# Kernel tuning notes

Measured on AMD Instinct MI355X. Metric: run time of the kernel, lower is better.

The kernel has to match this reference:

```python
import jax, jax.numpy as jnp
import numpy as np

TEMPS = (0.02, 0.05, 0.2)
EPS = 1e-06


def _pairwise_dist_sq(x, y):
    # (N, M) squared L2 distances, clamped at 0 like the torch version
    dsq = (x * x).sum(-1)[:, None] + (y * y).sum(-1)[None, :] - 2.0 * (x @ y.T)
    return jnp.maximum(dsq, 0.0)


def reference(gen_features, pos_features, drift_scales):
    gen, pos = gen_features, pos_features
    N = gen.shape[0]
    # Distances are temperature-independent; compute once and reuse across temps.
    d_att = jnp.sqrt(_pairwise_dist_sq(gen, pos))  # (N_gen, N_pos)
    eye = jnp.eye(N, dtype=bool)
    dsq_rep = _pairwise_dist_sq(gen, gen)
    # diagonal gets masked to -inf in the logits anyway; replace 0 before sqrt for numerical safety
    d_rep = jnp.sqrt(jnp.where(eye, 1.0, dsq_rep))  # (N_gen, N_gen)

    drift_sum = jnp.zeros_like(gen)
    for i, T in enumerate(TEMPS):
        # attraction: sum_j softmax(-d/T)_ij * (pos_j - gen_i) == softmax @ pos - gen
        # (weights sum to 1 along axis=1, so the -gen_i term factors out)
        w_att = jax.nn.softmax(-d_att / T, axis=1)
        attraction = w_att @ pos - gen
        # repulsion: self-pair excluded via -inf logit (masked_fill(inf) on distances)
        logits_rep = jnp.where(eye, -jnp.inf, -d_rep / T)
        w_rep = jax.nn.softmax(logits_rep, axis=1)
        repulsion = w_rep @ gen - gen
        scale = jnp.maximum(drift_scales[i], EPS)
        drift_sum = drift_sum + (attraction - repulsion) / scale
    return drift_sum / len(TEMPS)


def setup_inputs() -> dict:
    key = jax.random.key(0)
    k1, k2 = jax.random.split(key)
    return {
        "gen_features": jax.random.normal(k1, (8192, 1024), dtype=jnp.float32),
        "pos_features": jax.random.normal(k2, (8192, 1024), dtype=jnp.float32),
        "drift_scales": jnp.ones((3,), dtype=jnp.float32),
    }
```

## Files before the change

### kernel.cpp

```cpp
#include <hip/hip_runtime.h>
#include <hip/hip_bf16.h>

#define NN 8192
#define DD 1024
#define KK 16384

using half8 = __attribute__((ext_vector_type(8))) _Float16;
using half4 = __attribute__((ext_vector_type(4))) _Float16;
using f32x4 = __attribute__((ext_vector_type(4))) float;

__device__ __align__(16) _Float16 g_gh[(size_t)NN * DD];
__device__ __align__(16) _Float16 g_ph[(size_t)NN * DD];
__device__ __align__(16) _Float16 g_vt[(size_t)DD * KK];
__device__ float g_gn[NN];
__device__ float g_pn[NN];
__device__ float g_datt[(size_t)NN * NN];
__device__ float g_drep[(size_t)NN * NN];
__device__ __align__(16) _Float16 g_w[(size_t)NN * KK];
__device__ float g_part[2 * (size_t)NN * DD];

typedef const __attribute__((address_space(1))) void GV;
typedef __attribute__((address_space(3))) void LV;
__device__ inline void gload16(const void* g, void* l) {
    __builtin_amdgcn_global_load_lds((GV*)g, (LV*)l, 16, 0, 0);
}

__global__ __launch_bounds__(256) void k_conv(const float* __restrict__ gen,
                                              const float* __restrict__ pos) {
    int b = blockIdx.x;
    int r = b & (NN - 1);
    const float* src = (b < NN) ? gen : pos;
    _Float16* dsth = (b < NN) ? g_gh : g_ph;
    float* dstn = (b < NN) ? g_gn : g_pn;
    int t = threadIdx.x;
    const float4* s4 = (const float4*)(src + (size_t)r * DD);
    float4 x = s4[t];
    half4 h = {(_Float16)x.x, (_Float16)x.y, (_Float16)x.z, (_Float16)x.w};
    *(half4*)(dsth + (size_t)r * DD + t * 4) = h;
    float s = x.x * x.x + x.y * x.y + x.z * x.z + x.w * x.w;
#pragma unroll
    for (int off = 32; off; off >>= 1) s += __shfl_xor(s, off);
    __shared__ float red[4];
    if ((t & 63) == 0) red[t >> 6] = s;
    __syncthreads();
    if (t == 0) dstn[r] = red[0] + red[1] + red[2] + red[3];
}

__global__ __launch_bounds__(256) void k_tr(const float* __restrict__ pos,
                                            const float* __restrict__ gen) {
    int jt = blockIdx.x;
    int dt = blockIdx.y;
    int z = blockIdx.z;
    const float* src = z ? gen : pos;
    size_t cbase = z ? (size_t)NN : 0;
    __shared__ _Float16 tile[64][68];
    int t = threadIdx.x;
    int j0 = jt * 64, d0 = dt * 64;
#pragma unroll
    for (int p = 0; p < 4; p++) {
        int idx = t + p * 256;
        int r = idx >> 4;
        int c4 = idx & 15;
        float4 x = *(const float4*)(src + (size_t)(j0 + r) * DD + d0 + c4 * 4);
        tile[r][c4 * 4 + 0] = (_Float16)x.x;
        tile[r][c4 * 4 + 1] = (_Float16)x.y;
        tile[r][c4 * 4 + 2] = (_Float16)x.z;
        tile[r][c4 * 4 + 3] = (_Float16)x.w;
    }
    __syncthreads();
#pragma unroll
    for (int p = 0; p < 4; p++) {
        int idx = t + p * 256;
        int d = idx >> 4;
        int j4 = idx & 15;
        half4 h = {tile[j4 * 4 + 0][d], tile[j4 * 4 + 1][d],
                   tile[j4 * 4 + 2][d], tile[j4 * 4 + 3][d]};
        *(half4*)(g_vt + (size_t)(d0 + d) * KK + cbase + j0 + j4 * 4) = h;
    }
}

#define MFMA16(A_, B_, C_) __builtin_amdgcn_mfma_f32_16x16x32_f16(A_, B_, C_, 0, 0, 0)

template <int LDK>
__device__ inline void gemm_core(const _Float16* __restrict__ A,
                                 const _Float16* __restrict__ B,
                                 int arow0, int brow0, int kcol0, int ntiles,
                                 _Float16* lds, f32x4 acc[8][4]) {
    int t = threadIdx.x;
    int w = t >> 6, lane = t & 63;
    int wm = w >> 2, wn = w & 3;
    int q = lane >> 4, li = lane & 15;
    _Float16* sA = lds;
    _Float16* sB = lds + 4 * 8192;

    int offA[8], offB[4];
#pragma unroll
    for (int m = 0; m < 8; ++m) {
        int row = wm * 128 + m * 16 + li;
        offA[m] = row * 32 + (q ^ ((row >> 1) & 3)) * 8;
    }
#pragma unroll
    for (int n = 0; n < 4; ++n) {
        int row = wn * 64 + n * 16 + li;
        offB[n] = row * 32 + (q ^ ((row >> 1) & 3)) * 8;
    }

    int rbase = w * 16 + (lane >> 2);
    int csrc = (lane & 3) ^ ((rbase >> 1) & 3);
    const _Float16* gA0 = A + (size_t)(arow0 + rbase) * LDK + kcol0 + csrc * 8;
    const _Float16* gA1 = gA0 + (size_t)128 * LDK;
    const _Float16* gB0 = B + (size_t)(brow0 + rbase) * LDK + kcol0 + csrc * 8;
    const _Float16* gB1 = gB0 + (size_t)128 * LDK;
    int ldst = w * 512;

#pragma unroll
    for (int p = 0; p < 3; ++p) {
        gload16(gA0 + p * 32, sA + p * 8192 + ldst);
        gload16(gA1 + p * 32, sA + p * 8192 + 4096 + ldst);
        gload16(gB0 + p * 32, sB + p * 8192 + ldst);
        gload16(gB1 + p * 32, sB + p * 8192 + 4096 + ldst);
    }
    asm volatile("s_waitcnt vmcnt(4)" ::: "memory");
    __builtin_amdgcn_s_barrier();

    half8 af[4], bf[4], a2[4], afn[4], bfn[4];
#pragma unroll
    for (int m = 0; m < 4; ++m) af[m] = *(const half8*)(sA + offA[m]);
#pragma unroll
    for (int n = 0; n < 4; ++n) bf[n] = *(const half8*)(sB + offB[n]);

#pragma unroll 2
    for (int kt = 0; kt < ntiles; ++kt) {
        const _Float16* ca = sA + (kt & 3) * 8192;
        const _Float16* na = sA + ((kt + 1) & 3) * 8192;
        const _Float16* nb = sB + ((kt + 1) & 3) * 8192;
        if (kt + 3 < ntiles) {
            gload16(gA0 + (size_t)(kt + 3) * 32, sA + ((kt + 3) & 3) * 8192 + ldst);
            gload16(gA1 + (size_t)(kt + 3) * 32, sA + ((kt + 3) & 3) * 8192 + 4096 + ldst);
        }
#pragma unroll
        for (int m = 0; m < 4; ++m) a2[m] = *(const half8*)(ca + offA[m + 4]);
        if (kt + 1 < ntiles) {
#pragma unroll
            for (int m = 0; m < 4; ++m) afn[m] = *(const half8*)(na + offA[m]);
#pragma unroll
            for (int n = 0; n < 4; ++n) bfn[n] = *(const half8*)(nb + offB[n]);
        }
        __builtin_amdgcn_s_setprio(1);
#pragma unroll
        for (int m = 0; m < 4; ++m)
#pragma unroll
            for (int n = 0; n < 4; ++n)
                acc[m][n] = MFMA16(af[m], bf[n], acc[m][n]);
        __builtin_amdgcn_s_setprio(0);
        if (kt + 3 < ntiles) {
            gload16(gB0 + (size_t)(kt + 3) * 32, sB + ((kt + 3) & 3) * 8192 + ldst);
            gload16(gB1 + (size_t)(kt + 3) * 32, sB + ((kt + 3) & 3) * 8192 + 4096 + ldst);
        }
        __builtin_amdgcn_s_setprio(1);
#pragma unroll
        for (int m = 0; m < 4; ++m)
#pragma unroll
            for (int n = 0; n < 4; ++n)
                acc[m + 4][n] = MFMA16(a2[m], bf[n], acc[m + 4][n]);
        __builtin_amdgcn_s_setprio(0);
        if (kt + 1 < ntiles) {
#pragma unroll
            for (int m = 0; m < 4; ++m) af[m] = afn[m];
#pragma unroll
            for (int n = 0; n < 4; ++n) bf[n] = bfn[n];
        }
        if (kt < ntiles - 1) {
            if (kt + 3 < ntiles)
                asm volatile("s_waitcnt vmcnt(4)" ::: "memory");
            else
                asm volatile("s_waitcnt vmcnt(0)" ::: "memory");
            __builtin_amdgcn_s_barrier();
        }
    }
}

__global__ __launch_bounds__(512, 2) void k_qk2() {
    extern __shared__ _Float16 lds[];
    int id = blockIdx.y * 32 + blockIdx.x;
    id = (id & 7) * 128 + (id >> 3);
    int rt = id >> 5, ct = id & 31;
    int rep = blockIdx.z;
    const _Float16* A = g_gh;
    const _Float16* B = rep ? g_gh : g_ph;
    const float* An = g_gn;
    const float* Bn = rep ? g_gn : g_pn;
    float* outp = rep ? g_drep : g_datt;

    f32x4 acc[8][4] = {};
    gemm_core<DD>(A, B, rt * 256, ct * 256, 0, DD / 32, lds, acc);

    int t = threadIdx.x, w = t >> 6, lane = t & 63;
    int wm = w >> 2, wn = w & 3, q = lane >> 4, li = lane & 15;
    float bnv[4];
#pragma unroll
    for (int n = 0; n < 4; ++n) bnv[n] = Bn[ct * 256 + wn * 64 + n * 16 + li];
#pragma unroll
    for (int m = 0; m < 8; ++m) {
        int gi0 = rt * 256 + wm * 128 + m * 16 + q * 4;
#pragma unroll
        for (int r = 0; r < 4; ++r) {
            int gi = gi0 + r;
            float an = An[gi];
            float* orow = outp + (size_t)gi * NN;
#pragma unroll
            for (int n = 0; n < 4; ++n) {
                int gj = ct * 256 + wn * 64 + n * 16 + li;
                float dsq = an + bnv[n] - 2.0f * acc[m][n][r];
                float d = sqrtf(fmaxf(dsq, 0.0f));
                if (rep && gi == gj) d = 1e30f;
                orow[gj] = d;
            }
        }
    }
}

__global__ __launch_bounds__(256) void k_sw(const float* __restrict__ scales) {
    int i = blockIdx.x, t = threadIdx.x;
    const float4* ra = (const float4*)(g_datt + (size_t)i * NN);
    const float4* rr = (const float4*)(g_drep + (size_t)i * NN);
    float va[32], vr[32];
    float mna = 1e30f, mnr = 1e30f;
#pragma unroll
    for (int p = 0; p < 8; ++p) {
        float4 x = ra[t + p * 256];
        float4 y = rr[t + p * 256];
        va[p * 4 + 0] = x.x; va[p * 4 + 1] = x.y; va[p * 4 + 2] = x.z; va[p * 4 + 3] = x.w;
        vr[p * 4 + 0] = y.x; vr[p * 4 + 1] = y.y; vr[p * 4 + 2] = y.z; vr[p * 4 + 3] = y.w;
        mna = fminf(mna, fminf(fminf(x.x, x.y), fminf(x.z, x.w)));
        mnr = fminf(mnr, fminf(fminf(y.x, y.y), fminf(y.z, y.w)));
    }
#pragma unroll
    for (int off = 32; off; off >>= 1) {
        mna = fminf(mna, __shfl_xor(mna, off));
        mnr = fminf(mnr, __shfl_xor(mnr, off));
    }
    __shared__ float sm[2][4];
    __shared__ float ss[6][4];
    int wv = t >> 6;
    if ((t & 63) == 0) { sm[0][wv] = mna; sm[1][wv] = mnr; }
    __syncthreads();
    mna = fminf(fminf(sm[0][0], sm[0][1]), fminf(sm[0][2], sm[0][3]));
    mnr = fminf(fminf(sm[1][0], sm[1][1]), fminf(sm[1][2], sm[1][3]));
    float s0 = 0.f, s1 = 0.f, s2 = 0.f, s3 = 0.f, s4 = 0.f, s5 = 0.f;
#pragma unroll
    for (int k = 0; k < 32; ++k) {
        float da = va[k] - mna;
        s0 += __expf(da * -50.0f); s1 += __expf(da * -20.0f); s2 += __expf(da * -5.0f);
        float dr = vr[k] - mnr;
        s3 += __expf(dr * -50.0f); s4 += __expf(dr * -20.0f); s5 += __expf(dr * -5.0f);
    }
#pragma unroll
    for (int off = 32; off; off >>= 1) {
        s0 += __shfl_xor(s0, off); s1 += __shfl_xor(s1, off); s2 += __shfl_xor(s2, off);
        s3 += __shfl_xor(s3, off); s4 += __shfl_xor(s4, off); s5 += __shfl_xor(s5, off);
    }
    if ((t & 63) == 0) {
        ss[0][wv] = s0; ss[1][wv] = s1; ss[2][wv] = s2;
        ss[3][wv] = s3; ss[4][wv] = s4; ss[5][wv] = s5;
    }
    __syncthreads();
    float l0 = ss[0][0] + ss[0][1] + ss[0][2] + ss[0][3];
    float l1 = ss[1][0] + ss[1][1] + ss[1][2] + ss[1][3];
    float l2 = ss[2][0] + ss[2][1] + ss[2][2] + ss[2][3];
    float l3 = ss[3][0] + ss[3][1] + ss[3][2] + ss[3][3];
    float l4 = ss[4][0] + ss[4][1] + ss[4][2] + ss[4][3];
    float l5 = ss[5][0] + ss[5][1] + ss[5][2] + ss[5][3];
    float i0 = 1.0f / (3.0f * fmaxf(scales[0], 1e-6f));
    float i1 = 1.0f / (3.0f * fmaxf(scales[1], 1e-6f));
    float i2 = 1.0f / (3.0f * fmaxf(scales[2], 1e-6f));
    float ca0 = i0 / l0, ca1 = i1 / l1, ca2 = i2 / l2;
    float cr0 = -i0 / l3, cr1 = -i1 / l4, cr2 = -i2 / l5;
    _Float16* wa = g_w + (size_t)i * KK;
    _Float16* wr = wa + NN;
#pragma unroll
    for (int p = 0; p < 8; ++p) {
        half4 ha, hr;
#pragma unroll
        for (int qq = 0; qq < 4; ++qq) {
            float da = va[p * 4 + qq] - mna;
            ha[qq] = (_Float16)(ca0 * __expf(da * -50.0f) + ca1 * __expf(da * -20.0f) +
                                ca2 * __expf(da * -5.0f));
            float dr = vr[p * 4 + qq] - mnr;
            hr[qq] = (_Float16)(cr0 * __expf(dr * -50.0f) + cr1 * __expf(dr * -20.0f) +
                                cr2 * __expf(dr * -5.0f));
        }
        *(half4*)(wa + (size_t)(t + p * 256) * 4) = ha;
        *(half4*)(wr + (size_t)(t + p * 256) * 4) = hr;
    }
}

__global__ __launch_bounds__(512, 2) void k_gemm2() {
    extern __shared__ _Float16 lds[];
    int id = blockIdx.y * 4 + blockIdx.x;
    id = (id & 7) * 16 + (id >> 3);
    int rt = id >> 2, ct = id & 3;
    int z = blockIdx.z;
    f32x4 acc[8][4] = {};
    gemm_core<KK>(g_w, g_vt, rt * 256, ct * 256, z * (KK / 2), (KK / 2) / 32, lds, acc);
    float* outp = g_part + (size_t)z * NN * DD;
    int t = threadIdx.x, w = t >> 6, lane = t & 63;
    int wm = w >> 2, wn = w & 3, q = lane >> 4, li = lane & 15;
#pragma unroll
    for (int m = 0; m < 8; ++m) {
#pragma unroll
        for (int r = 0; r < 4; ++r) {
            int gi = rt * 256 + wm * 128 + m * 16 + q * 4 + r;
            float* orow = outp + (size_t)gi * DD;
#pragma unroll
            for (int n = 0; n < 4; ++n) {
                int gj = ct * 256 + wn * 64 + n * 16 + li;
                orow[gj] = acc[m][n][r];
            }
        }
    }
}

__global__ __launch_bounds__(256) void k_red(float* __restrict__ out) {
    size_t base = (size_t)blockIdx.x * 256 + threadIdx.x;
    const float4* p0 = (const float4*)g_part;
    const float4* p1 = (const float4*)(g_part + (size_t)NN * DD);
    float4* o4 = (float4*)out;
#pragma unroll
    for (int p = 0; p < 4; ++p) {
        size_t idx = base + (size_t)p * 524288;
        float4 a = p0[idx], b = p1[idx];
        float4 c = {a.x + b.x, a.y + b.y, a.z + b.z, a.w + b.w};
        o4[idx] = c;
    }
}

extern "C" void kernel_launch(void* const* d_in, const int* in_sizes, int n_in,
                              void* d_out, int out_size, void* d_ws, size_t ws_size,
                              hipStream_t stream) {
    (void)in_sizes; (void)n_in; (void)d_ws; (void)ws_size; (void)out_size;
    const float* gen = (const float*)d_in[0];
    const float* pos = (const float*)d_in[1];
    const float* scales = (const float*)d_in[2];

    hipFuncSetAttribute((const void*)k_qk2, hipFuncAttributeMaxDynamicSharedMemorySize, 131072);
    hipFuncSetAttribute((const void*)k_gemm2, hipFuncAttributeMaxDynamicSharedMemorySize, 131072);

    k_conv<<<dim3(2 * NN), 256, 0, stream>>>(gen, pos);
    k_tr<<<dim3(128, 16, 2), 256, 0, stream>>>(pos, gen);
    k_qk2<<<dim3(32, 32, 2), 512, 131072, stream>>>();
    k_sw<<<dim3(NN), 256, 0, stream>>>(scales);
    k_gemm2<<<dim3(4, 32, 2), 512, 131072, stream>>>();
    k_red<<<dim3(2048), 256, 0, stream>>>((float*)d_out);
}
```

Measured before the change: 919.2 us.

## Restructure GEMM mainloop into ping-pong phases with explicit barriers

Rewrites the shared GEMM mainloop from a 3-deep prefetch with register double-buffering of fragments into a 2-tile window. Each tile is split into two half-tile phases, and each phase loads its LDS fragments, issues global loads, hits a barrier, waits on lgkmcnt, then runs its MFMAs. The goal is to coordinate waves so memory and MFMA phases alternate and register pressure drops. The cost is many more block-wide barriers per k-tile and less lookahead in the prefetch. It also assumes ntiles is even.

```diff
diff --git a/kernel.cpp b/kernel.cpp
--- a/kernel.cpp
+++ b/kernel.cpp
@@ -80,6 +80,11 @@
 }
 
 #define MFMA16(A_, B_, C_) __builtin_amdgcn_mfma_f32_16x16x32_f16(A_, B_, C_, 0, 0, 0)
+#define BAR() __builtin_amdgcn_s_barrier()
+#define LGKM0() do { asm volatile("s_waitcnt lgkmcnt(0)" ::: "memory"); \
+                     __builtin_amdgcn_sched_barrier(0); } while (0)
+#define VM4() asm volatile("s_waitcnt vmcnt(4)" ::: "memory")
+#define VM0() asm volatile("s_waitcnt vmcnt(0)" ::: "memory")
 
 template <int LDK>
 __device__ inline void gemm_core(const _Float16* __restrict__ A,
@@ -113,39 +118,33 @@
     const _Float16* gB1 = gB0 + (size_t)128 * LDK;
     int ldst = w * 512;
 
-#pragma unroll
-    for (int p = 0; p < 3; ++p) {
-        gload16(gA0 + p * 32, sA + p * 8192 + ldst);
-        gload16(gA1 + p * 32, sA + p * 8192 + 4096 + ldst);
-        gload16(gB0 + p * 32, sB + p * 8192 + ldst);
-        gload16(gB1 + p * 32, sB + p * 8192 + 4096 + ldst);
-    }
-    asm volatile("s_waitcnt vmcnt(4)" ::: "memory");
-    __builtin_amdgcn_s_barrier();
-
-    half8 af[4], bf[4], a2[4], afn[4], bfn[4];
-#pragma unroll
-    for (int m = 0; m < 4; ++m) af[m] = *(const half8*)(sA + offA[m]);
-#pragma unroll
-    for (int n = 0; n < 4; ++n) bf[n] = *(const half8*)(sB + offB[n]);
-
+#define STAGE_A(tile_) do { \
+    gload16(gA0 + (size_t)(tile_) * 32, sA + ((tile_) & 3) * 8192 + ldst); \
+    gload16(gA1 + (size_t)(tile_) * 32, sA + ((tile_) & 3) * 8192 + 4096 + ldst); } while (0)
+#define STAGE_B(tile_) do { \
+    gload16(gB0 + (size_t)(tile_) * 32, sB + ((tile_) & 3) * 8192 + ldst); \
+    gload16(gB1 + (size_t)(tile_) * 32, sB + ((tile_) & 3) * 8192 + 4096 + ldst); } while (0)
+
+    STAGE_A(0); STAGE_B(0); STAGE_A(1); STAGE_B(1);
+    VM4();
+    BAR();
+
+    int nwin = ntiles >> 1;
+    half8 af[4], bf[4], af2[4];
 #pragma unroll 2
-    for (int kt = 0; kt < ntiles; ++kt) {
-        const _Float16* ca = sA + (kt & 3) * 8192;
-        const _Float16* na = sA + ((kt + 1) & 3) * 8192;
-        const _Float16* nb = sB + ((kt + 1) & 3) * 8192;
-        if (kt + 3 < ntiles) {
-            gload16(gA0 + (size_t)(kt + 3) * 32, sA + ((kt + 3) & 3) * 8192 + ldst);
-            gload16(gA1 + (size_t)(kt + 3) * 32, sA + ((kt + 3) & 3) * 8192 + 4096 + ldst);
-        }
-#pragma unroll
-        for (int m = 0; m < 4; ++m) a2[m] = *(const half8*)(ca + offA[m + 4]);
-        if (kt + 1 < ntiles) {
-#pragma unroll
-            for (int m = 0; m < 4; ++m) afn[m] = *(const half8*)(na + offA[m]);
-#pragma unroll
-            for (int n = 0; n < 4; ++n) bfn[n] = *(const half8*)(nb + offB[n]);
-        }
+    for (int wi = 0; wi < nwin; ++wi) {
+        int t0 = 2 * wi, t1 = t0 + 1;
+        const _Float16* a0 = sA + (t0 & 3) * 8192;
+        const _Float16* b0 = sB + (t0 & 3) * 8192;
+        const _Float16* a1 = sA + (t1 & 3) * 8192;
+        const _Float16* b1 = sB + (t1 & 3) * 8192;
+#pragma unroll
+        for (int m = 0; m < 4; ++m) af[m] = *(const half8*)(a0 + offA[m]);
+#pragma unroll
+        for (int n = 0; n < 4; ++n) bf[n] = *(const half8*)(b0 + offB[n]);
+        if (t0 + 2 < ntiles) STAGE_A(t0 + 2);
+        BAR();
+        LGKM0();
         __builtin_amdgcn_s_setprio(1);
 #pragma unroll
         for (int m = 0; m < 4; ++m)
@@ -153,31 +152,55 @@
             for (int n = 0; n < 4; ++n)
                 acc[m][n] = MFMA16(af[m], bf[n], acc[m][n]);
         __builtin_amdgcn_s_setprio(0);
-        if (kt + 3 < ntiles) {
-            gload16(gB0 + (size_t)(kt + 3) * 32, sB + ((kt + 3) & 3) * 8192 + ldst);
-            gload16(gB1 + (size_t)(kt + 3) * 32, sB + ((kt + 3) & 3) * 8192 + 4096 + ldst);
+        BAR();
+#pragma unroll
+        for (int m = 0; m < 4; ++m) af2[m] = *(const half8*)(a0 + offA[m + 4]);
+        if (t0 + 2 < ntiles) STAGE_B(t0 + 2);
+        BAR();
+        LGKM0();
+        __builtin_amdgcn_s_setprio(1);
+#pragma unroll
+        for (int m = 0; m < 4; ++m)
+#pragma unroll
+            for (int n = 0; n < 4; ++n)
+                acc[m + 4][n] = MFMA16(af2[m], bf[n], acc[m + 4][n]);
+        __builtin_amdgcn_s_setprio(0);
+        if (wi < nwin - 1) VM4(); else VM0();
+        BAR();
+#pragma unroll
+        for (int m = 0; m < 4; ++m) af[m] = *(const half8*)(a1 + offA[m]);
+#pragma unroll
+        for (int n = 0; n < 4; ++n) bf[n] = *(const half8*)(b1 + offB[n]);
+        if (t1 + 2 < ntiles) STAGE_A(t1 + 2);
+        BAR();
+        LGKM0();
+        __builtin_amdgcn_s_setprio(1);
+#pragma unroll
+        for (int m = 0; m < 4; ++m)
+#pragma unroll
+            for (int n = 0; n < 4; ++n)
+                acc[m][n] = MFMA16(af[m], bf[n], acc[m][n]);
+        __builtin_amdgcn_s_setprio(0);
+        BAR();
+#pragma unroll
+        for (int m = 0; m < 4; ++m) af2[m] = *(const half8*)(a1 + offA[m + 4]);
+        if (t1 + 2 < ntiles) STAGE_B(t1 + 2);
+        BAR();
+        LGKM0();
+        __builtin_amdgcn_s_setprio(1);
+#pragma unroll
+        for (int m = 0; m < 4; ++m)
+#pragma unroll
+            for (int n = 0; n < 4; ++n)
+                acc[m + 4][n] = MFMA16(af2[m], bf[n], acc[m + 4][n]);
+        __builtin_amdgcn_s_setprio(0);
+        if (wi < nwin - 1) {
+            VM4();
+            BAR();
         }
-        __builtin_amdgcn_s_setprio(1);
-#pragma unroll
-        for (int m = 0; m < 4; ++m)
-#pragma unroll
-            for (int n = 0; n < 4; ++n)
-                acc[m + 4][n] = MFMA16(a2[m], bf[n], acc[m + 4][n]);
-        __builtin_amdgcn_s_setprio(0);
-        if (kt + 1 < ntiles) {
-#pragma unroll
-            for (int m = 0; m < 4; ++m) af[m] = afn[m];
-#pragma unroll
-            for (int n = 0; n < 4; ++n) bf[n] = bfn[n];
-        }
-        if (kt < ntiles - 1) {
-            if (kt + 3 < ntiles)
-                asm volatile("s_waitcnt vmcnt(4)" ::: "memory");
-            else
-                asm volatile("s_waitcnt vmcnt(0)" ::: "memory");
-            __builtin_amdgcn_s_barrier();
-        }
-    }
+    }
+#undef STAGE_A
+#undef STAGE_B
 }
 
 __global__ __launch_bounds__(512, 2) void k_qk2() {
```

New measurement: 898.3 us. 2.3% less time.
